# Optimization experiments

Hardware: AMD Instinct MI355X
Metric: run time of the kernel (lower is better)

## Reference

```python
import jax, jax.numpy as jnp
import numpy as np
from jax import lax

D_MODEL = 1024
EXPAND = 2
D_INNER = EXPAND * D_MODEL          # 2048
HEADDIM = 64
NHEADS = D_INNER // HEADDIM         # 32
D_STATE = 128
D_CONV = 4
NGROUPS = 1
CONV_DIM = D_INNER + 2 * NGROUPS * D_STATE   # 2304
D_IN_PROJ = 2 * D_INNER + 2 * NGROUPS * D_STATE + NHEADS  # 4384
EPS = 1e-5
BSZ, SEQ = 4, 1024


def _layer_norm(x):
    mu = jnp.mean(x, -1, keepdims=True)
    v = jnp.var(x, -1, keepdims=True)
    return (x - mu) * lax.rsqrt(v + EPS)


def _smart_flip(X, mask):
    # reverse only the non-padded prefix of each sequence
    B, L, _ = X.shape
    lengths = jnp.sum(~mask, axis=1)                     # (B,)
    r = jnp.arange(L)[None, :]                           # (1,L)
    pos = jnp.where(r < lengths[:, None], lengths[:, None] - 1 - r, r)
    return jnp.take_along_axis(X, pos[:, :, None], axis=1)


def _mamba2(u, in_proj_w, conv_w, conv_b, dt_bias, A_log, D, norm_w, out_proj_w):
    B, L, _ = u.shape
    zxbcdt = jnp.einsum('bld,ed->ble', u, in_proj_w)     # (B,L,D_IN_PROJ)
    z = zxbcdt[..., :D_INNER]
    xBC = zxbcdt[..., D_INNER:D_INNER + CONV_DIM]
    dt = zxbcdt[..., D_INNER + CONV_DIM:]                # (B,L,H)
    dt = jax.nn.softplus(dt + dt_bias)
    # causal depthwise conv1d over time, then SiLU
    xc = jnp.transpose(xBC, (0, 2, 1))                   # (B,C,L)
    xc = jnp.pad(xc, ((0, 0), (0, 0), (D_CONV - 1, 0)))
    xc = lax.conv_general_dilated(xc, conv_w.reshape(CONV_DIM, 1, D_CONV), (1,), 'VALID',
                                  feature_group_count=CONV_DIM)
    xBC = jax.nn.silu(jnp.transpose(xc + conv_b[None, :, None], (0, 2, 1)))
    x = xBC[..., :D_INNER].reshape(B, L, NHEADS, HEADDIM)
    Bmat = xBC[..., D_INNER:D_INNER + D_STATE]           # (B,L,N)  (ngroups=1)
    Cmat = xBC[..., D_INNER + D_STATE:]                  # (B,L,N)
    A = -jnp.exp(A_log)                                  # (H,)
    dA = jnp.exp(dt * A)                                 # (B,L,H)

    def step(h, inp):
        dA_t, dt_t, x_t, B_t, C_t = inp
        # h: (B,H,P,N)
        h = h * dA_t[:, :, None, None] + (dt_t[:, :, None] * x_t)[..., None] * B_t[:, None, None, :]
        y = jnp.einsum('bhpn,bn->bhp', h, C_t)
        return h, y

    h0 = jnp.zeros((B, NHEADS, HEADDIM, D_STATE), u.dtype)
    xs = (jnp.moveaxis(dA, 1, 0), jnp.moveaxis(dt, 1, 0), jnp.moveaxis(x, 1, 0),
          jnp.moveaxis(Bmat, 1, 0), jnp.moveaxis(Cmat, 1, 0))
    _, ys = lax.scan(step, h0, xs)                       # (L,B,H,P)
    y = jnp.moveaxis(ys, 0, 1) + D[None, None, :, None] * x
    y = y.reshape(B, L, D_INNER)
    g = y * jax.nn.silu(z)                               # gated RMSNorm (norm_before_gate=False)
    y = g * lax.rsqrt(jnp.mean(g * g, -1, keepdims=True) + EPS) * norm_w
    return jnp.einsum('ble,de->bld', y, out_proj_w)


def setup_inputs() -> dict:
    key = jax.random.key(0)
    ks = jax.random.split(key, 16)
    dt_f = jax.random.uniform(ks[4], (NHEADS,), minval=0.001, maxval=0.1)
    dt_r = jax.random.uniform(ks[10], (NHEADS,), minval=0.001, maxval=0.1)
    inv_softplus = lambda d: d + jnp.log(-jnp.expm1(-d))
    return {
        'hidden_states': jax.random.normal(ks[0], (BSZ, SEQ, D_MODEL), jnp.float32),
        'src_key_padding_mask': jnp.zeros((BSZ, SEQ), jnp.bool_),
        'in_proj_w': jax.random.normal(ks[1], (D_IN_PROJ, D_MODEL), jnp.float32) / np.sqrt(D_MODEL),
        'out_proj_w': jax.random.normal(ks[2], (D_MODEL, D_INNER), jnp.float32) / np.sqrt(D_INNER),
        'conv_w_f': jax.random.normal(ks[3], (CONV_DIM, D_CONV), jnp.float32) / np.sqrt(D_CONV),
        'conv_b_f': jnp.zeros((CONV_DIM,), jnp.float32),
        'dt_bias_f': inv_softplus(dt_f),
        'A_log_f': jnp.log(jax.random.uniform(ks[5], (NHEADS,), minval=1.0, maxval=16.0)),
        'D_f': jnp.ones((NHEADS,), jnp.float32),
        'norm_w_f': jnp.ones((D_INNER,), jnp.float32),
        'conv_w_r': jax.random.normal(ks[9], (CONV_DIM, D_CONV), jnp.float32) / np.sqrt(D_CONV),
        'conv_b_r': jnp.zeros((CONV_DIM,), jnp.float32),
        'dt_bias_r': inv_softplus(dt_r),
        'A_log_r': jnp.log(jax.random.uniform(ks[11], (NHEADS,), minval=1.0, maxval=16.0)),
        'D_r': jnp.ones((NHEADS,), jnp.float32),
        'norm_w_r': jnp.ones((D_INNER,), jnp.float32),
    }


def reference(hidden_states, src_key_padding_mask, in_proj_w, out_proj_w,
              conv_w_f, conv_b_f, dt_bias_f, A_log_f, D_f, norm_w_f,
              conv_w_r, conv_b_r, dt_bias_r, A_log_r, D_r, norm_w_r):
    h = _layer_norm(hidden_states)
    out = _mamba2(h, in_proj_w, conv_w_f, conv_b_f, dt_bias_f, A_log_f, D_f, norm_w_f, out_proj_w)
    rev = _smart_flip(h, src_key_padding_mask)
    out_rev = _mamba2(rev, in_proj_w, conv_w_r, conv_b_r, dt_bias_r, A_log_r, D_r, norm_w_r, out_proj_w)
    out_rev = _smart_flip(out_rev, src_key_padding_mask)
    out = (out + out_rev) / 2
    return _layer_norm(out)
```

## Files before the change

### kernel.cpp

```cpp
#include <hip/hip_runtime.h>


#define BSZ 4
#define SEQ 1024
#define DMODEL 1024
#define DINNER 2048
#define NHEADS 32
#define HEADDIM 64
#define DSTATE 128
#define CONVDIM 2304
#define DPROJ 4384
#define DPROJ_PAD 4480
#define NTOK (BSZ*SEQ)
#define EPSF 1e-5f
#define CH 32
#define NCHK (SEQ/CH)

typedef float f32x4 __attribute__((ext_vector_type(4)));
typedef __bf16 bf16x8 __attribute__((ext_vector_type(8)));

__device__ __forceinline__ unsigned short f2bf(float f) {
  unsigned int x = __float_as_uint(f);
  unsigned int r = (x + 0x7fffu + ((x >> 16) & 1u)) >> 16;
  return (unsigned short)r;
}
__device__ __forceinline__ float bf2f(unsigned short u) {
  return __uint_as_float(((unsigned int)u) << 16);
}

__device__ __forceinline__ void async_load16(const void* g, void* l) {
  __builtin_amdgcn_global_load_lds(
      (const __attribute__((address_space(1))) void*)g,
      (__attribute__((address_space(3))) void*)l, 16, 0, 0);
}

#define W1N (DPROJ_PAD * DMODEL)
#define W2N (DMODEL * DINNER)
__global__ void k_convert(const float* __restrict__ w1, const float* __restrict__ w2,
                          unsigned short* __restrict__ o1, unsigned short* __restrict__ o2) {
  int idx = blockIdx.x * 256 + threadIdx.x;
  if (idx < W1N) {
    int row = idx >> 10, col = idx & 1023;
    float v = (row < DPROJ) ? w1[(size_t)row * DMODEL + col] : 0.f;
    o1[idx] = f2bf(v);
  } else {
    int k = idx - W1N;
    o2[k] = f2bf(w2[k]);
  }
}
__global__ void k_lengths(const unsigned char* __restrict__ mask, int* __restrict__ lengths) {
  int b = blockIdx.x, tid = threadIdx.x;
  int cnt = 0;
  for (int k = 0; k < 4; ++k)
    cnt += (mask[(size_t)b * SEQ + tid + k * 256] == 0) ? 1 : 0;
  for (int o = 32; o > 0; o >>= 1) cnt += __shfl_down(cnt, o);
  __shared__ int red[4];
  if ((tid & 63) == 0) red[tid >> 6] = cnt;
  __syncthreads();
  if (tid == 0) lengths[b] = red[0] + red[1] + red[2] + red[3];
}

__global__ __launch_bounds__(256) void k_ln_bf16(const float* __restrict__ in,
                                                 unsigned short* __restrict__ out) {
  int row = blockIdx.x, tid = threadIdx.x;
  float4 v = ((const float4*)(in + (size_t)row * DMODEL))[tid];
  float s = v.x + v.y + v.z + v.w;
  float ss = v.x * v.x + v.y * v.y + v.z * v.z + v.w * v.w;
  for (int o = 32; o > 0; o >>= 1) { s += __shfl_down(s, o); ss += __shfl_down(ss, o); }
  __shared__ float red[8];
  if ((tid & 63) == 0) { red[tid >> 6] = s; red[4 + (tid >> 6)] = ss; }
  __syncthreads();
  s = red[0] + red[1] + red[2] + red[3];
  ss = red[4] + red[5] + red[6] + red[7];
  float mu = s * (1.f / DMODEL);
  float var = ss * (1.f / DMODEL) - mu * mu;
  float rs = rsqrtf(var + EPSF);
  ushort4 o;
  o.x = f2bf((v.x - mu) * rs); o.y = f2bf((v.y - mu) * rs);
  o.z = f2bf((v.z - mu) * rs); o.w = f2bf((v.w - mu) * rs);
  ((ushort4*)(out + (size_t)row * DMODEL))[tid] = o;
}

__global__ __launch_bounds__(256) void k_ln_f32(const float* __restrict__ in,
                                                float* __restrict__ out) {
  int row = blockIdx.x, tid = threadIdx.x;
  float4 v = ((const float4*)(in + (size_t)row * DMODEL))[tid];
  float s = v.x + v.y + v.z + v.w;
  float ss = v.x * v.x + v.y * v.y + v.z * v.z + v.w * v.w;
  for (int o = 32; o > 0; o >>= 1) { s += __shfl_down(s, o); ss += __shfl_down(ss, o); }
  __shared__ float red[8];
  if ((tid & 63) == 0) { red[tid >> 6] = s; red[4 + (tid >> 6)] = ss; }
  __syncthreads();
  s = red[0] + red[1] + red[2] + red[3];
  ss = red[4] + red[5] + red[6] + red[7];
  float mu = s * (1.f / DMODEL);
  float var = ss * (1.f / DMODEL) - mu * mu;
  float rs = rsqrtf(var + EPSF);
  float4 o;
  o.x = (v.x - mu) * rs; o.y = (v.y - mu) * rs;
  o.z = (v.z - mu) * rs; o.w = (v.w - mu) * rs;
  ((float4*)(out + (size_t)row * DMODEL))[tid] = o;
}

__global__ __launch_bounds__(256) void k_gemm_bt(const unsigned short* __restrict__ A,
                                                 const unsigned short* __restrict__ B,
                                                 float* __restrict__ C,
                                                 int K, int lda, int ldb, int ldc) {
  __shared__ unsigned short Asm[128 * 32];
  __shared__ unsigned short Bsm[128 * 32];
  const int tid = threadIdx.x;
  const int lane = tid & 63;
  const int w = tid >> 6;
  const int wm = w >> 1, wn = w & 1;
  const long m0 = (long)blockIdx.x * 128;
  const long n0 = (long)blockIdx.y * 128;

  const int sr = lane >> 2;
  const int sc = (lane & 3) * 8;
  const unsigned short* gA0 = A + (m0 + (w * 2 + 0) * 16 + sr) * (long)lda + sc;
  const unsigned short* gA1 = A + (m0 + (w * 2 + 1) * 16 + sr) * (long)lda + sc;
  const unsigned short* gB0 = B + (n0 + (w * 2 + 0) * 16 + sr) * (long)ldb + sc;
  const unsigned short* gB1 = B + (n0 + (w * 2 + 1) * 16 + sr) * (long)ldb + sc;
  unsigned short* lA0 = Asm + (w * 2 + 0) * 512;
  unsigned short* lA1 = Asm + (w * 2 + 1) * 512;
  unsigned short* lB0 = Bsm + (w * 2 + 0) * 512;
  unsigned short* lB1 = Bsm + (w * 2 + 1) * 512;

  f32x4 acc[4][4] = {};
  const int q8 = (lane >> 4) * 8;
  const int r16 = lane & 15;

  for (int k0 = 0; k0 < K; k0 += 32) {
    async_load16(gA0 + k0, lA0);
    async_load16(gA1 + k0, lA1);
    async_load16(gB0 + k0, lB0);
    async_load16(gB1 + k0, lB1);
    __syncthreads();
    bf16x8 af[4], bfr[4];
#pragma unroll
    for (int i = 0; i < 4; ++i)
      af[i] = *reinterpret_cast<const bf16x8*>(Asm + (wm * 64 + i * 16 + r16) * 32 + q8);
#pragma unroll
    for (int j = 0; j < 4; ++j)
      bfr[j] = *reinterpret_cast<const bf16x8*>(Bsm + (wn * 64 + j * 16 + r16) * 32 + q8);
#pragma unroll
    for (int i = 0; i < 4; ++i)
#pragma unroll
      for (int j = 0; j < 4; ++j)
        acc[i][j] = __builtin_amdgcn_mfma_f32_16x16x32_bf16(af[i], bfr[j], acc[i][j], 0, 0, 0);
    __syncthreads();
  }
  const int q = lane >> 4, cn = lane & 15;
#pragma unroll
  for (int i = 0; i < 4; ++i)
#pragma unroll
    for (int j = 0; j < 4; ++j) {
      long crow = m0 + wm * 64 + i * 16 + q * 4;
      long ccol = n0 + wn * 64 + j * 16 + cn;
#pragma unroll
      for (int r = 0; r < 4; ++r)
        C[(crow + r) * (long)ldc + ccol] = acc[i][j][r];
    }
}

__global__ __launch_bounds__(256) void k_conv(
    const float* __restrict__ zx,
    const float* __restrict__ cw_f, const float* __restrict__ cb_f,
    const float* __restrict__ cw_r, const float* __restrict__ cb_r,
    const int* __restrict__ lengths,
    __bf16* __restrict__ xb) {
  const int bx = blockIdx.x;
  const int tg = bx & 63;
  const int db = bx >> 6;
  const int b = db & 3;
  const int dir = db >> 2;
  const int tid = threadIdx.x;
  const int len = lengths[b];
  const int t0 = tg * 16;

  const float* cw = dir ? cw_r : cw_f;
  const float* cb = dir ? cb_r : cb_f;

  float w0[9], w1[9], w2[9], w3[9], bias[9];
  float r0[9], r1[9], r2[9], r3[9];
#pragma unroll
  for (int k = 0; k < 9; ++k) {
    int c = tid + k * 256;
    float4 w4 = *(const float4*)(cw + (size_t)c * 4);
    w0[k] = w4.x; w1[k] = w4.y; w2[k] = w4.z; w3[k] = w4.w;
    bias[k] = cb[c];
    r0[k] = 0.f; r1[k] = 0.f; r2[k] = 0.f;
  }
  auto rowptr = [&](int tt) -> const float* {
    int s = dir ? ((tt < len) ? (len - 1 - tt) : tt) : tt;
    return zx + ((size_t)b * SEQ + s) * DPROJ_PAD + DINNER;
  };
  if (t0 >= 3) {
    const float* ra = rowptr(t0 - 3);
    const float* rb = rowptr(t0 - 2);
    const float* rc = rowptr(t0 - 1);
#pragma unroll
    for (int k = 0; k < 9; ++k) {
      int c = tid + k * 256;
      r0[k] = ra[c]; r1[k] = rb[c]; r2[k] = rc[c];
    }
  }
  {
    const float* rp = rowptr(t0);
#pragma unroll
    for (int k = 0; k < 9; ++k) r3[k] = rp[tid + k * 256];
  }
  for (int j = 0; j < 16; ++j) {
    float r4[9];
    if (j < 15) {
      const float* rp = rowptr(t0 + j + 1);
#pragma unroll
      for (int k = 0; k < 9; ++k) r4[k] = rp[tid + k * 256];
    }
    __bf16* orow = xb + ((size_t)db * SEQ + t0 + j) * CONVDIM;
#pragma unroll
    for (int k = 0; k < 9; ++k) {
      float acc = bias[k];
      acc = fmaf(w0[k], r0[k], acc);
      acc = fmaf(w1[k], r1[k], acc);
      acc = fmaf(w2[k], r2[k], acc);
      acc = fmaf(w3[k], r3[k], acc);
      float sig = 1.f / (1.f + __expf(-acc));
      orow[tid + k * 256] = (__bf16)(acc * sig);
      r0[k] = r1[k]; r1[k] = r2[k]; r2[k] = r3[k]; r3[k] = r4[k];
    }
  }
}

__global__ __launch_bounds__(256) void k_dtprep(
    const float* __restrict__ zx,
    const float* __restrict__ dtb_f, const float* __restrict__ dtb_r,
    const float* __restrict__ al_f, const float* __restrict__ al_r,
    const int* __restrict__ lengths, float* __restrict__ ddg) {
  const int task = (blockIdx.x * 256 + threadIdx.x) >> 5;
  const int l32 = threadIdx.x & 31;
  const int chunk = task & 31, hh = (task >> 5) & 31, db = task >> 10;
  const int b = db & 3, dir = db >> 2;
  const int len = lengths[b];
  const float dtbv = (dir ? dtb_r : dtb_f)[hh];
  const float Ah = -__expf((dir ? al_r : al_f)[hh]);
  const int s = chunk * 32 + l32;
  const int sf = dir ? ((s < len) ? (len - 1 - s) : s) : s;
  float raw = zx[(size_t)(b * SEQ + sf) * DPROJ_PAD + DINNER + CONVDIM + hh] + dtbv;
  float d = (raw > 20.f) ? raw : log1pf(__expf(raw));
  float cum = d;
#pragma unroll
  for (int o = 1; o < 32; o <<= 1) {
    float v = __shfl_up(cum, o, 32);
    if (l32 >= o) cum += v;
  }
  float cum31 = __shfl(cum, 31, 32);
  float* o = ddg + (size_t)task * 128;
  o[l32]      = d;
  o[32 + l32] = Ah * cum;
  o[64 + l32] = d * __expf(Ah * (cum31 - cum));
  o[96 + l32] = __expf(Ah * cum);
}

__global__ __launch_bounds__(256) void k_scan(
    const __bf16* __restrict__ xb, const float* __restrict__ ddg,
    const float* __restrict__ D_f, const float* __restrict__ D_r,
    unsigned short* __restrict__ y) {
  __shared__ __bf16 Crawf[2][4096];
  __shared__ __bf16 Brawf[2][4096];
  __shared__ __bf16 Braw2[2][4096];
  __shared__ __bf16 BTf[4096];
  __shared__ float  ddL[2][128];
  __shared__ __bf16 SL[1024];
  __shared__ __bf16 HL[4][2048];
  __shared__ __bf16 yO[2][32 * 72];

  const int bx = blockIdx.x;
  const int h = bx & 31;
  const int db = bx >> 5;
  const int dir = db >> 2;
  const int tid = threadIdx.x;
  const int lane = tid & 63;
  const int w = tid >> 6;
  const int l15 = lane & 15;
  const int q = lane >> 4;

  const float Dh = (dir ? D_r : D_f)[h];
  const __bf16* xbase = xb + (size_t)db * SEQ * CONVDIM;
  const float* ddbase = ddg + (size_t)bx * NCHK * 128;
  unsigned short* ybase = y + (size_t)db * SEQ * DINNER + h * HEADDIM;

  for (int i = lane; i < 2048; i += 64) HL[w][i] = (__bf16)0.f;
  for (int i = tid; i < 1024; i += 256) SL[i] = (__bf16)0.f;

  f32x4 accH[8] = {};

  auto issue = [&](int c, int nb) {
    const __bf16* xr = xbase + (size_t)c * CH * CONVDIM;
#pragma unroll
    for (int k = 0; k < 2; ++k) {
      const int idx = w * 2 + k;
      const int P = idx * 64 + lane;
      const int tt = P >> 8, kk = (P >> 6) & 3, qq = (P >> 4) & 3, ll = P & 15;
      const __bf16* gB = xr + (size_t)(tt * 16 + ll) * CONVDIM + DINNER + kk * 32 + qq * 8;
      async_load16(gB, &Brawf[nb][idx * 512]);
      async_load16(gB + 128, &Crawf[nb][idx * 512]);
      const int s = P >> 4, n8 = P & 15;
      const __bf16* g2 = xr + (size_t)s * CONVDIM + DINNER + n8 * 8;
      async_load16(g2, &Braw2[nb][idx * 512]);
    }
    if (w == 3 && lane < 32)
      async_load16(ddbase + (size_t)c * 128 + lane * 4, &ddL[nb][0]);
  };

  auto load_xt = [&](int c) {
    bf16x8 v;
    const __bf16* gx = xbase + (size_t)(c * CH + q * 8) * CONVDIM + h * HEADDIM + w * 16 + l15;
#pragma unroll
    for (int j = 0; j < 8; ++j) v[j] = gx[(size_t)j * CONVDIM];
    return v;
  };

  issue(0, 0);
  bf16x8 xt = load_xt(0);
  __syncthreads();

  for (int c = 0; c < NCHK; ++c) {
    const int cb = c & 1, nb = cb ^ 1;

    if (c > 0) {
      const int tf = tid >> 3, p8 = (tid & 7) * 8;
      bf16x8 vy = *(const bf16x8*)&yO[nb][tf * 72 + p8];
      *(bf16x8*)(ybase + (size_t)((c - 1) * CH + tf) * DINNER + p8) = vy;
    }

    {
      const int n = tid & 127, sg = tid >> 7;
#pragma unroll
      for (int e = 0; e < 2; ++e) {
        const int qp = sg * 2 + e;
        bf16x8 v;
#pragma unroll
        for (int j = 0; j < 8; ++j) v[j] = Braw2[cb][(qp * 8 + j) * 128 + n];
        *(bf16x8*)&BTf[((n >> 4) * 64 + qp * 16 + (n & 15)) * 8] = v;
      }
    }

    bf16x8 Cf0[4], Cf1[4];
#pragma unroll
    for (int kk = 0; kk < 4; ++kk) {
      Cf0[kk] = *(const bf16x8*)&Crawf[cb][(kk * 64 + lane) * 8];
      Cf1[kk] = *(const bf16x8*)&Crawf[cb][((4 + kk) * 64 + lane) * 8];
    }
    if (w < 3) {
      const int tt = (w == 0) ? 0 : 1;
      const int ss = (w == 2) ? 1 : 0;
      f32x4 G = {};
#pragma unroll
      for (int kk = 0; kk < 4; ++kk) {
        bf16x8 Bq = *(const bf16x8*)&Brawf[cb][((ss * 4 + kk) * 64 + lane) * 8];
        G = __builtin_amdgcn_mfma_f32_16x16x32_bf16(tt ? Cf1[kk] : Cf0[kk], Bq, G, 0, 0, 0);
      }
      const int sgl = ss * 16 + l15;
      const float sdt = ddL[cb][sgl];
      const float scd = ddL[cb][32 + sgl];
#pragma unroll
      for (int r = 0; r < 4; ++r) {
        const int t0 = q * 4 + r;
        float v = G[r] * sdt * __expf(ddL[cb][32 + tt * 16 + t0] - scd);
        if (tt == ss) {
          if (t0 < l15) v = 0.f;
          else if (t0 == l15) v += Dh;
        }
        SL[(tt * 64 + (ss * 2 + (l15 >> 3)) * 16 + t0) * 8 + (l15 & 7)] = (__bf16)v;
      }
    }
    __syncthreads();

    if (c + 1 < NCHK) issue(c + 1, nb);
    bf16x8 xt_n;
    if (c + 1 < NCHK) xt_n = load_xt(c + 1);

    f32x4 accy0 = {}, accy1 = {};
    {
      bf16x8 S0 = *(const bf16x8*)&SL[(lane) * 8];
      bf16x8 S1 = *(const bf16x8*)&SL[(64 + lane) * 8];
      accy0 = __builtin_amdgcn_mfma_f32_16x16x32_bf16(xt, S0, accy0, 0, 0, 0);
      accy1 = __builtin_amdgcn_mfma_f32_16x16x32_bf16(xt, S1, accy1, 0, 0, 0);
    }
    {
      f32x4 ai0 = {}, ai1 = {};
#pragma unroll
      for (int kk = 0; kk < 4; ++kk) {
        bf16x8 Hf = *(const bf16x8*)&HL[w][(kk * 64 + lane) * 8];
        ai0 = __builtin_amdgcn_mfma_f32_16x16x32_bf16(Hf, Cf0[kk], ai0, 0, 0, 0);
        ai1 = __builtin_amdgcn_mfma_f32_16x16x32_bf16(Hf, Cf1[kk], ai1, 0, 0, 0);
      }
      const float P0 = ddL[cb][96 + l15], P1 = ddL[cb][96 + 16 + l15];
      accy0 = accy0 + ai0 * P0;
      accy1 = accy1 + ai1 * P1;
    }
    {
      const float atot = ddL[cb][96 + 31];
      bf16x8 xw;
#pragma unroll
      for (int j = 0; j < 8; ++j)
        xw[j] = (__bf16)((float)xt[j] * ddL[cb][64 + q * 8 + j]);
#pragma unroll
      for (int nt = 0; nt < 8; ++nt) {
        bf16x8 Bt = *(const bf16x8*)&BTf[(nt * 64 + lane) * 8];
        accH[nt] = accH[nt] * atot;
        accH[nt] = __builtin_amdgcn_mfma_f32_16x16x32_bf16(xw, Bt, accH[nt], 0, 0, 0);
      }
#pragma unroll
      for (int nt = 0; nt < 8; ++nt)
#pragma unroll
        for (int r = 0; r < 4; ++r) {
          const int n = nt * 16 + l15;
          HL[w][((n >> 5) * 64 + ((n & 31) >> 3) * 16 + q * 4 + r) * 8 + (n & 7)] =
              (__bf16)accH[nt][r];
        }
    }
#pragma unroll
    for (int r = 0; r < 4; ++r) {
      const int p = w * 16 + q * 4 + r;
      yO[cb][l15 * 72 + p]        = (__bf16)accy0[r];
      yO[cb][(16 + l15) * 72 + p] = (__bf16)accy1[r];
    }
    xt = xt_n;
    __syncthreads();
  }
  {
    const int tf = tid >> 3, p8 = (tid & 7) * 8;
    bf16x8 vy = *(const bf16x8*)&yO[(NCHK - 1) & 1][tf * 72 + p8];
    *(bf16x8*)(ybase + (size_t)((NCHK - 1) * CH + tf) * DINNER + p8) = vy;
  }
}

__global__ __launch_bounds__(256) void k_gate_combine(
    const float* __restrict__ zx, const unsigned short* __restrict__ y,
    const float* __restrict__ nw_f, const float* __restrict__ nw_r,
    const int* __restrict__ lengths, unsigned short* __restrict__ comb) {
  const int bx = blockIdx.x;
  const int b = bx >> 10, l = bx & 1023;
  const int tid = threadIdx.x;
  const int len = lengths[b];
  const int pos = (l < len) ? (len - 1 - l) : l;
  const float* z = zx + (size_t)bx * DPROJ_PAD;
  const unsigned short* yf = y + ((size_t)b * SEQ + l) * DINNER;
  const unsigned short* yr = y + ((size_t)(BSZ + b) * SEQ + pos) * DINNER;

  float gf[8], gr[8];
  float sf = 0.f, sr = 0.f;
#pragma unroll
  for (int k = 0; k < 8; ++k) {
    int c = tid + k * 256;
    float zz = z[c];
    float sz = zz / (1.f + __expf(-zz));
    float vf = bf2f(yf[c]) * sz;
    float vr = bf2f(yr[c]) * sz;
    gf[k] = vf; gr[k] = vr;
    sf += vf * vf; sr += vr * vr;
  }
  for (int o = 32; o > 0; o >>= 1) { sf += __shfl_down(sf, o); sr += __shfl_down(sr, o); }
  __shared__ float red[8];
  if ((tid & 63) == 0) { red[tid >> 6] = sf; red[4 + (tid >> 6)] = sr; }
  __syncthreads();
  sf = red[0] + red[1] + red[2] + red[3];
  sr = red[4] + red[5] + red[6] + red[7];
  float rf = rsqrtf(sf * (1.f / DINNER) + EPSF);
  float rr = rsqrtf(sr * (1.f / DINNER) + EPSF);
#pragma unroll
  for (int k = 0; k < 8; ++k) {
    int c = tid + k * 256;
    float o = 0.5f * (gf[k] * rf * nw_f[c] + gr[k] * rr * nw_r[c]);
    comb[(size_t)bx * DINNER + c] = f2bf(o);
  }
}

extern "C" void kernel_launch(void* const* d_in, const int* in_sizes, int n_in,
                              void* d_out, int out_size, void* d_ws, size_t ws_size,
                              hipStream_t stream) {
  const float* hidden      = (const float*)d_in[0];
  const unsigned char* msk = (const unsigned char*)d_in[1];
  const float* in_proj_w   = (const float*)d_in[2];
  const float* out_proj_w  = (const float*)d_in[3];
  const float* conv_w_f    = (const float*)d_in[4];
  const float* conv_b_f    = (const float*)d_in[5];
  const float* dt_bias_f   = (const float*)d_in[6];
  const float* A_log_f     = (const float*)d_in[7];
  const float* D_f         = (const float*)d_in[8];
  const float* norm_w_f    = (const float*)d_in[9];
  const float* conv_w_r    = (const float*)d_in[10];
  const float* conv_b_r    = (const float*)d_in[11];
  const float* dt_bias_r   = (const float*)d_in[12];
  const float* A_log_r     = (const float*)d_in[13];
  const float* D_r         = (const float*)d_in[14];
  const float* norm_w_r    = (const float*)d_in[15];
  float* outF = (float*)d_out;

  char* ws = (char*)d_ws;
  size_t o_w1b  = 0;
  size_t o_w2b  = o_w1b  + 9175040;
  size_t o_hb   = o_w2b  + 4194304;
  size_t o_zx   = o_hb   + 8388608;
  size_t o_xb   = o_zx   + 73400320;
  size_t o_dd   = o_xb   + 37748736;
  size_t o_y    = o_dd   + 4194304;
  size_t o_comb = o_y    + 33554432;
  size_t o_outp = o_comb + 16777216;
  size_t o_len  = o_outp + 16777216;

  unsigned short* W1b  = (unsigned short*)(ws + o_w1b);
  unsigned short* W2b  = (unsigned short*)(ws + o_w2b);
  unsigned short* hb   = (unsigned short*)(ws + o_hb);
  float*          zx   = (float*)(ws + o_zx);
  __bf16*         xb   = (__bf16*)(ws + o_xb);
  float*          ddg  = (float*)(ws + o_dd);
  unsigned short* yB   = (unsigned short*)(ws + o_y);
  unsigned short* comb = (unsigned short*)(ws + o_comb);
  float*          outp = (float*)(ws + o_outp);
  int*            lens = (int*)(ws + o_len);

  k_convert<<<(W1N + W2N) / 256, 256, 0, stream>>>(in_proj_w, out_proj_w, W1b, W2b);
  k_lengths<<<BSZ, 256, 0, stream>>>(msk, lens);

  k_ln_bf16<<<NTOK, 256, 0, stream>>>(hidden, hb);

  k_gemm_bt<<<dim3(NTOK / 128, DPROJ_PAD / 128), 256, 0, stream>>>(
      hb, W1b, zx, DMODEL, DMODEL, DMODEL, DPROJ_PAD);

  k_conv<<<2 * BSZ * (SEQ / 16), 256, 0, stream>>>(
      zx, conv_w_f, conv_b_f, conv_w_r, conv_b_r, lens, xb);

  k_dtprep<<<1024, 256, 0, stream>>>(
      zx, dt_bias_f, dt_bias_r, A_log_f, A_log_r, lens, ddg);

  k_scan<<<2 * BSZ * NHEADS, 256, 0, stream>>>(xb, ddg, D_f, D_r, yB);

  k_gate_combine<<<NTOK, 256, 0, stream>>>(zx, yB, norm_w_f, norm_w_r, lens, comb);

  k_gemm_bt<<<dim3(NTOK / 128, DMODEL / 128), 256, 0, stream>>>(
      comb, W2b, outp, DINNER, DINNER, DINNER, DMODEL);

  k_ln_f32<<<NTOK, 256, 0, stream>>>(outp, outF);

  (void)in_sizes; (void)n_in; (void)out_size; (void)ws_size;
}
```

Measured before the change: 347.4 us.

## Store in_proj output as bf16 and single-buffer scan shared memory

The in_proj GEMM gets a bf16-output variant, so the large zxbcdt intermediate is written and then read back by conv, dtprep and gate_combine at half the bytes. The workspace slot for it shrinks to match. Separately, the scan kernel drops the double-buffered B/C staging arrays in LDS and adds launch_bounds(256,2), aiming for two resident blocks per CU. The trade-offs are lower precision in z, xBC and dt before the conv and softplus, and possible loss of load/compute overlap in the scan, or a buffer race if prefetches still target the buffer currently being read.

Result: faster. 327.2 us (-5.8%).

```diff
diff --git a/kernel.cpp b/kernel.cpp
--- a/kernel.cpp
+++ b/kernel.cpp
@@ -102,55 +102,55 @@
   ((float4*)(out + (size_t)row * DMODEL))[tid] = o;
 }
 
+#define GEMM_BODY                                                              \
+  __shared__ unsigned short Asm[128 * 32];                                     \
+  __shared__ unsigned short Bsm[128 * 32];                                     \
+  const int tid = threadIdx.x;                                                 \
+  const int lane = tid & 63;                                                   \
+  const int w = tid >> 6;                                                      \
+  const int wm = w >> 1, wn = w & 1;                                           \
+  const long m0 = (long)blockIdx.x * 128;                                      \
+  const long n0 = (long)blockIdx.y * 128;                                      \
+  const int sr = lane >> 2;                                                    \
+  const int sc = (lane & 3) * 8;                                               \
+  const unsigned short* gA0 = A + (m0 + (w * 2 + 0) * 16 + sr) * (long)lda + sc; \
+  const unsigned short* gA1 = A + (m0 + (w * 2 + 1) * 16 + sr) * (long)lda + sc; \
+  const unsigned short* gB0 = B + (n0 + (w * 2 + 0) * 16 + sr) * (long)ldb + sc; \
+  const unsigned short* gB1 = B + (n0 + (w * 2 + 1) * 16 + sr) * (long)ldb + sc; \
+  unsigned short* lA0 = Asm + (w * 2 + 0) * 512;                               \
+  unsigned short* lA1 = Asm + (w * 2 + 1) * 512;                               \
+  unsigned short* lB0 = Bsm + (w * 2 + 0) * 512;                               \
+  unsigned short* lB1 = Bsm + (w * 2 + 1) * 512;                               \
+  f32x4 acc[4][4] = {};                                                        \
+  const int q8 = (lane >> 4) * 8;                                              \
+  const int r16 = lane & 15;                                                   \
+  for (int k0 = 0; k0 < K; k0 += 32) {                                         \
+    async_load16(gA0 + k0, lA0);                                               \
+    async_load16(gA1 + k0, lA1);                                               \
+    async_load16(gB0 + k0, lB0);                                               \
+    async_load16(gB1 + k0, lB1);                                               \
+    __syncthreads();                                                           \
+    bf16x8 af[4], bfr[4];                                                      \
+    _Pragma("unroll")                                                          \
+    for (int i = 0; i < 4; ++i)                                                \
+      af[i] = *reinterpret_cast<const bf16x8*>(Asm + (wm * 64 + i * 16 + r16) * 32 + q8); \
+    _Pragma("unroll")                                                          \
+    for (int j = 0; j < 4; ++j)                                                \
+      bfr[j] = *reinterpret_cast<const bf16x8*>(Bsm + (wn * 64 + j * 16 + r16) * 32 + q8); \
+    _Pragma("unroll")                                                          \
+    for (int i = 0; i < 4; ++i)                                                \
+      _Pragma("unroll")                                                        \
+      for (int j = 0; j < 4; ++j)                                              \
+        acc[i][j] = __builtin_amdgcn_mfma_f32_16x16x32_bf16(af[i], bfr[j], acc[i][j], 0, 0, 0); \
+    __syncthreads();                                                           \
+  }                                                                            \
+  const int q = lane >> 4, cn = lane & 15;
+
 __global__ __launch_bounds__(256) void k_gemm_bt(const unsigned short* __restrict__ A,
                                                  const unsigned short* __restrict__ B,
                                                  float* __restrict__ C,
                                                  int K, int lda, int ldb, int ldc) {
-  __shared__ unsigned short Asm[128 * 32];
-  __shared__ unsigned short Bsm[128 * 32];
-  const int tid = threadIdx.x;
-  const int lane = tid & 63;
-  const int w = tid >> 6;
-  const int wm = w >> 1, wn = w & 1;
-  const long m0 = (long)blockIdx.x * 128;
-  const long n0 = (long)blockIdx.y * 128;
-
-  const int sr = lane >> 2;
-  const int sc = (lane & 3) * 8;
-  const unsigned short* gA0 = A + (m0 + (w * 2 + 0) * 16 + sr) * (long)lda + sc;
-  const unsigned short* gA1 = A + (m0 + (w * 2 + 1) * 16 + sr) * (long)lda + sc;
-  const unsigned short* gB0 = B + (n0 + (w * 2 + 0) * 16 + sr) * (long)ldb + sc;
-  const unsigned short* gB1 = B + (n0 + (w * 2 + 1) * 16 + sr) * (long)ldb + sc;
-  unsigned short* lA0 = Asm + (w * 2 + 0) * 512;
-  unsigned short* lA1 = Asm + (w * 2 + 1) * 512;
-  unsigned short* lB0 = Bsm + (w * 2 + 0) * 512;
-  unsigned short* lB1 = Bsm + (w * 2 + 1) * 512;
-
-  f32x4 acc[4][4] = {};
-  const int q8 = (lane >> 4) * 8;
-  const int r16 = lane & 15;
-
-  for (int k0 = 0; k0 < K; k0 += 32) {
-    async_load16(gA0 + k0, lA0);
-    async_load16(gA1 + k0, lA1);
-    async_load16(gB0 + k0, lB0);
-    async_load16(gB1 + k0, lB1);
-    __syncthreads();
-    bf16x8 af[4], bfr[4];
-#pragma unroll
-    for (int i = 0; i < 4; ++i)
-      af[i] = *reinterpret_cast<const bf16x8*>(Asm + (wm * 64 + i * 16 + r16) * 32 + q8);
-#pragma unroll
-    for (int j = 0; j < 4; ++j)
-      bfr[j] = *reinterpret_cast<const bf16x8*>(Bsm + (wn * 64 + j * 16 + r16) * 32 + q8);
-#pragma unroll
-    for (int i = 0; i < 4; ++i)
-#pragma unroll
-      for (int j = 0; j < 4; ++j)
-        acc[i][j] = __builtin_amdgcn_mfma_f32_16x16x32_bf16(af[i], bfr[j], acc[i][j], 0, 0, 0);
-    __syncthreads();
-  }
-  const int q = lane >> 4, cn = lane & 15;
+  GEMM_BODY
 #pragma unroll
   for (int i = 0; i < 4; ++i)
 #pragma unroll
@@ -163,8 +163,25 @@
     }
 }
 
+__global__ __launch_bounds__(256) void k_gemm_bt_h(const unsigned short* __restrict__ A,
+                                                   const unsigned short* __restrict__ B,
+                                                   unsigned short* __restrict__ C,
+                                                   int K, int lda, int ldb, int ldc) {
+  GEMM_BODY
+#pragma unroll
+  for (int i = 0; i < 4; ++i)
+#pragma unroll
+    for (int j = 0; j < 4; ++j) {
+      long crow = m0 + wm * 64 + i * 16 + q * 4;
+      long ccol = n0 + wn * 64 + j * 16 + cn;
+#pragma unroll
+      for (int r = 0; r < 4; ++r)
+        C[(crow + r) * (long)ldc + ccol] = f2bf(acc[i][j][r]);
+    }
+}
+
 __global__ __launch_bounds__(256) void k_conv(
-    const float* __restrict__ zx,
+    const __bf16* __restrict__ zxb,
     const float* __restrict__ cw_f, const float* __restrict__ cb_f,
     const float* __restrict__ cw_r, const float* __restrict__ cb_r,
     const int* __restrict__ lengths,
@@ -191,31 +208,31 @@
     bias[k] = cb[c];
     r0[k] = 0.f; r1[k] = 0.f; r2[k] = 0.f;
   }
-  auto rowptr = [&](int tt) -> const float* {
+  auto rowptr = [&](int tt) -> const __bf16* {
     int s = dir ? ((tt < len) ? (len - 1 - tt) : tt) : tt;
-    return zx + ((size_t)b * SEQ + s) * DPROJ_PAD + DINNER;
+    return zxb + ((size_t)b * SEQ + s) * DPROJ_PAD + DINNER;
   };
   if (t0 >= 3) {
-    const float* ra = rowptr(t0 - 3);
-    const float* rb = rowptr(t0 - 2);
-    const float* rc = rowptr(t0 - 1);
+    const __bf16* ra = rowptr(t0 - 3);
+    const __bf16* rb = rowptr(t0 - 2);
+    const __bf16* rc = rowptr(t0 - 1);
 #pragma unroll
     for (int k = 0; k < 9; ++k) {
       int c = tid + k * 256;
-      r0[k] = ra[c]; r1[k] = rb[c]; r2[k] = rc[c];
+      r0[k] = (float)ra[c]; r1[k] = (float)rb[c]; r2[k] = (float)rc[c];
     }
   }
   {
-    const float* rp = rowptr(t0);
-#pragma unroll
-    for (int k = 0; k < 9; ++k) r3[k] = rp[tid + k * 256];
+    const __bf16* rp = rowptr(t0);
+#pragma unroll
+    for (int k = 0; k < 9; ++k) r3[k] = (float)rp[tid + k * 256];
   }
   for (int j = 0; j < 16; ++j) {
     float r4[9];
     if (j < 15) {
-      const float* rp = rowptr(t0 + j + 1);
-#pragma unroll
-      for (int k = 0; k < 9; ++k) r4[k] = rp[tid + k * 256];
+      const __bf16* rp = rowptr(t0 + j + 1);
+#pragma unroll
+      for (int k = 0; k < 9; ++k) r4[k] = (float)rp[tid + k * 256];
     }
     __bf16* orow = xb + ((size_t)db * SEQ + t0 + j) * CONVDIM;
 #pragma unroll
@@ -233,7 +250,7 @@
 }
 
 __global__ __launch_bounds__(256) void k_dtprep(
-    const float* __restrict__ zx,
+    const __bf16* __restrict__ zxb,
     const float* __restrict__ dtb_f, const float* __restrict__ dtb_r,
     const float* __restrict__ al_f, const float* __restrict__ al_r,
     const int* __restrict__ lengths, float* __restrict__ ddg) {
@@ -246,7 +263,7 @@
   const float Ah = -__expf((dir ? al_r : al_f)[hh]);
   const int s = chunk * 32 + l32;
   const int sf = dir ? ((s < len) ? (len - 1 - s) : s) : s;
-  float raw = zx[(size_t)(b * SEQ + sf) * DPROJ_PAD + DINNER + CONVDIM + hh] + dtbv;
+  float raw = (float)zxb[(size_t)(b * SEQ + sf) * DPROJ_PAD + DINNER + CONVDIM + hh] + dtbv;
   float d = (raw > 20.f) ? raw : log1pf(__expf(raw));
   float cum = d;
 #pragma unroll
@@ -262,13 +279,13 @@
   o[96 + l32] = __expf(Ah * cum);
 }
 
-__global__ __launch_bounds__(256) void k_scan(
+__global__ __launch_bounds__(256, 2) void k_scan(
     const __bf16* __restrict__ xb, const float* __restrict__ ddg,
     const float* __restrict__ D_f, const float* __restrict__ D_r,
     unsigned short* __restrict__ y) {
-  __shared__ __bf16 Crawf[2][4096];
-  __shared__ __bf16 Brawf[2][4096];
-  __shared__ __bf16 Braw2[2][4096];
+  __shared__ __bf16 Crawf[4096];
+  __shared__ __bf16 Brawf[4096];
+  __shared__ __bf16 Braw2[4096];
   __shared__ __bf16 BTf[4096];
   __shared__ float  ddL[2][128];
   __shared__ __bf16 SL[1024];
@@ -303,11 +320,11 @@
       const int P = idx * 64 + lane;
       const int tt = P >> 8, kk = (P >> 6) & 3, qq = (P >> 4) & 3, ll = P & 15;
       const __bf16* gB = xr + (size_t)(tt * 16 + ll) * CONVDIM + DINNER + kk * 32 + qq * 8;
-      async_load16(gB, &Brawf[nb][idx * 512]);
-      async_load16(gB + 128, &Crawf[nb][idx * 512]);
+      async_load16(gB, &Brawf[idx * 512]);
+      async_load16(gB + 128, &Crawf[idx * 512]);
       const int s = P >> 4, n8 = P & 15;
       const __bf16* g2 = xr + (size_t)s * CONVDIM + DINNER + n8 * 8;
-      async_load16(g2, &Braw2[nb][idx * 512]);
+      async_load16(g2, &Braw2[idx * 512]);
     }
     if (w == 3 && lane < 32)
       async_load16(ddbase + (size_t)c * 128 + lane * 4, &ddL[nb][0]);
@@ -341,7 +358,7 @@
         const int qp = sg * 2 + e;
         bf16x8 v;
 #pragma unroll
-        for (int j = 0; j < 8; ++j) v[j] = Braw2[cb][(qp * 8 + j) * 128 + n];
+        for (int j = 0; j < 8; ++j) v[j] = Braw2[(qp * 8 + j) * 128 + n];
         *(bf16x8*)&BTf[((n >> 4) * 64 + qp * 16 + (n & 15)) * 8] = v;
       }
     }
@@ -349,8 +366,8 @@
     bf16x8 Cf0[4], Cf1[4];
 #pragma unroll
     for (int kk = 0; kk < 4; ++kk) {
-      Cf0[kk] = *(const bf16x8*)&Crawf[cb][(kk * 64 + lane) * 8];
-      Cf1[kk] = *(const bf16x8*)&Crawf[cb][((4 + kk) * 64 + lane) * 8];
+      Cf0[kk] = *(const bf16x8*)&Crawf[(kk * 64 + lane) * 8];
+      Cf1[kk] = *(const bf16x8*)&Crawf[((4 + kk) * 64 + lane) * 8];
     }
     if (w < 3) {
       const int tt = (w == 0) ? 0 : 1;
@@ -358,7 +375,7 @@
       f32x4 G = {};
 #pragma unroll
       for (int kk = 0; kk < 4; ++kk) {
-        bf16x8 Bq = *(const bf16x8*)&Brawf[cb][((ss * 4 + kk) * 64 + lane) * 8];
+        bf16x8 Bq = *(const bf16x8*)&Brawf[((ss * 4 + kk) * 64 + lane) * 8];
         G = __builtin_amdgcn_mfma_f32_16x16x32_bf16(tt ? Cf1[kk] : Cf0[kk], Bq, G, 0, 0, 0);
       }
       const int sgl = ss * 16 + l15;
@@ -438,7 +455,7 @@
 }
 
 __global__ __launch_bounds__(256) void k_gate_combine(
-    const float* __restrict__ zx, const unsigned short* __restrict__ y,
+    const __bf16* __restrict__ zxb, const unsigned short* __restrict__ y,
     const float* __restrict__ nw_f, const float* __restrict__ nw_r,
     const int* __restrict__ lengths, unsigned short* __restrict__ comb) {
   const int bx = blockIdx.x;
@@ -446,7 +463,7 @@
   const int tid = threadIdx.x;
   const int len = lengths[b];
   const int pos = (l < len) ? (len - 1 - l) : l;
-  const float* z = zx + (size_t)bx * DPROJ_PAD;
+  const __bf16* z = zxb + (size_t)bx * DPROJ_PAD;
   const unsigned short* yf = y + ((size_t)b * SEQ + l) * DINNER;
   const unsigned short* yr = y + ((size_t)(BSZ + b) * SEQ + pos) * DINNER;
 
@@ -455,7 +472,7 @@
 #pragma unroll
   for (int k = 0; k < 8; ++k) {
     int c = tid + k * 256;
-    float zz = z[c];
+    float zz = (float)z[c];
     float sz = zz / (1.f + __expf(-zz));
     float vf = bf2f(yf[c]) * sz;
     float vr = bf2f(yr[c]) * sz;
@@ -504,7 +521,7 @@
   size_t o_w2b  = o_w1b  + 9175040;
   size_t o_hb   = o_w2b  + 4194304;
   size_t o_zx   = o_hb   + 8388608;
-  size_t o_xb   = o_zx   + 73400320;
+  size_t o_xb   = o_zx   + 36700160;
   size_t o_dd   = o_xb   + 37748736;
   size_t o_y    = o_dd   + 4194304;
   size_t o_comb = o_y    + 33554432;
@@ -514,7 +531,7 @@
   unsigned short* W1b  = (unsigned short*)(ws + o_w1b);
   unsigned short* W2b  = (unsigned short*)(ws + o_w2b);
   unsigned short* hb   = (unsigned short*)(ws + o_hb);
-  float*          zx   = (float*)(ws + o_zx);
+  __bf16*         zxb  = (__bf16*)(ws + o_zx);
   __bf16*         xb   = (__bf16*)(ws + o_xb);
   float*          ddg  = (float*)(ws + o_dd);
   unsigned short* yB   = (unsigned short*)(ws + o_y);
@@ -527,18 +544,18 @@
 
   k_ln_bf16<<<NTOK, 256, 0, stream>>>(hidden, hb);
 
-  k_gemm_bt<<<dim3(NTOK / 128, DPROJ_PAD / 128), 256, 0, stream>>>(
-      hb, W1b, zx, DMODEL, DMODEL, DMODEL, DPROJ_PAD);
+  k_gemm_bt_h<<<dim3(NTOK / 128, DPROJ_PAD / 128), 256, 0, stream>>>(
+      hb, W1b, (unsigned short*)zxb, DMODEL, DMODEL, DMODEL, DPROJ_PAD);
 
   k_conv<<<2 * BSZ * (SEQ / 16), 256, 0, stream>>>(
-      zx, conv_w_f, conv_b_f, conv_w_r, conv_b_r, lens, xb);
+      zxb, conv_w_f, conv_b_f, conv_w_r, conv_b_r, lens, xb);
 
   k_dtprep<<<1024, 256, 0, stream>>>(
-      zx, dt_bias_f, dt_bias_r, A_log_f, A_log_r, lens, ddg);
+      zxb, dt_bias_f, dt_bias_r, A_log_f, A_log_r, lens, ddg);
 
   k_scan<<<2 * BSZ * NHEADS, 256, 0, stream>>>(xb, ddg, D_f, D_r, yB);
 
-  k_gate_combine<<<NTOK, 256, 0, stream>>>(zx, yB, norm_w_f, norm_w_r, lens, comb);
+  k_gate_combine<<<NTOK, 256, 0, stream>>>(zxb, yB, norm_w_f, norm_w_r, lens, comb);
 
   k_gemm_bt<<<dim3(NTOK / 128, DMODEL / 128), 256, 0, stream>>>(
       comb, W2b, outp, DINNER, DINNER, DINNER, DMODEL);
```
